# Kernel tuning notes

Hardware: AMD Instinct MI355X
Metric: run time of the kernel (lower is better)

Reference implementation:

```python
import jax, jax.numpy as jnp
import numpy as np

NEG_SLOPE = 0.2  # PyG GATConv default negative_slope


def setup_inputs() -> dict:
    key = jax.random.key(0)
    ks = jax.random.split(key, 10)
    B, N, E = 8, 10000, 160000
    Din, Dout = 128, 128
    x = jax.random.normal(ks[0], (B, N, Din), dtype=jnp.float32)
    src = jax.random.randint(ks[1], (E,), 0, N)
    dst = jax.random.randint(ks[2], (E,), 0, N)
    edge_index = jnp.stack([src, dst])  # [2, E]
    edge_attr = jax.random.uniform(ks[3], (E,), dtype=jnp.float32)
    lim = 1.0 / np.sqrt(Din)
    W = jax.random.uniform(ks[4], (Dout, Din), jnp.float32, -lim, lim)   # shared lin (src==dst)
    We = jax.random.uniform(ks[5], (Dout, 1), jnp.float32, -1.0, 1.0)    # lin_edge, edge_dim=1
    att_src = jax.random.normal(ks[6], (Dout,), jnp.float32) * 0.1
    att_dst = jax.random.normal(ks[7], (Dout,), jnp.float32) * 0.1
    att_edge = jax.random.normal(ks[8], (Dout,), jnp.float32) * 0.1
    bias = jnp.zeros((Dout,), jnp.float32)
    return {"x": x, "edge_index": edge_index, "edge_attr": edge_attr,
            "W": W, "We": We, "att_src": att_src, "att_dst": att_dst,
            "att_edge": att_edge, "bias": bias}


def reference(x, edge_index, edge_attr, W, We, att_src, att_dst, att_edge, bias):
    B, N, Din = x.shape
    src, dst = edge_index[0], edge_index[1]
    # --- add self loops with fill_value='mean' (mean of incoming edge_attr per node) ---
    deg = jax.ops.segment_sum(jnp.ones_like(edge_attr), dst, num_segments=N)
    loop_attr = jax.ops.segment_sum(edge_attr, dst, num_segments=N) / jnp.maximum(deg, 1.0)
    ar = jnp.arange(N, dtype=src.dtype)
    full_src = jnp.concatenate([src, ar])          # [E2]
    full_dst = jnp.concatenate([dst, ar])          # [E2]
    full_attr = jnp.concatenate([edge_attr, loop_attr])
    # edge features: Linear(1 -> Dout, no bias) == outer product; identical across batch
    e_feat = full_attr[:, None] * We[:, 0][None, :]        # [E2, Dout]
    alpha_e = e_feat @ att_edge                            # [E2]

    def single(xb):  # xb: [N, Din]
        h = xb @ W.T                                       # [N, Dout]
        a_src = h @ att_src                                # [N]
        a_dst = h @ att_dst                                # [N]
        a = a_src[full_src] + a_dst[full_dst] + alpha_e    # [E2]
        a = jax.nn.leaky_relu(a, NEG_SLOPE)
        # segment softmax over destination node
        a_max = jax.ops.segment_max(a, full_dst, num_segments=N)
        a_max = jnp.where(jnp.isfinite(a_max), a_max, 0.0)
        ex = jnp.exp(a - a_max[full_dst])
        s = jax.ops.segment_sum(ex, full_dst, num_segments=N)
        alpha = ex / (s[full_dst] + 1e-16)                 # [E2]
        out = jax.ops.segment_sum(alpha[:, None] * h[full_src], full_dst, num_segments=N)
        return out + bias, alpha

    x_out, attn = jax.vmap(single)(x)   # [B, N, Dout], [B, E2]
    return x_out, attn
```

## Files before the change

### kernel.cpp

```cpp
#include <hip/hip_runtime.h>
#include <hip/hip_bf16.h>
#include <hip/hip_fp16.h>

typedef short short8 __attribute__((ext_vector_type(8)));
typedef float floatx4 __attribute__((ext_vector_type(4)));

static constexpr int BATCH = 8;
static constexpr int NN    = 10000;
static constexpr int EE    = 160000;
static constexpr int EE2   = EE + NN;
static constexpr int DD    = 128;
static constexpr int STR   = 64;
static constexpr float SLOPE = 0.2f;
static constexpr long OUT_ELEMS = (long)BATCH * NN * DD;
static constexpr int EB = EE / 256;

__device__ inline float ldf(const void* p, long i, int f32) {
    return f32 ? ((const float*)p)[i]
               : __bfloat162float(((const __hip_bfloat16*)p)[i]);
}
__device__ inline int esrc(const int* ei, int e, int i64) { return i64 ? ei[2 * e] : ei[e]; }
__device__ inline int edst(const int* ei, int e, int i64) { return i64 ? ei[2 * (EE + e)] : ei[EE + e]; }
__device__ inline short bf16bits(float v) {
    __hip_bfloat16 b = __float2bfloat16(v);
    short s; __builtin_memcpy(&s, &b, 2); return s;
}
__device__ inline short f16bits(float v) {
    __half b = __float2half(v);
    short s; __builtin_memcpy(&s, &b, 2); return s;
}

__global__ __launch_bounds__(256) void k_detect(const unsigned short* __restrict__ xu,
                                                const int* __restrict__ ei,
                                                const void* __restrict__ We,
                                                const void* __restrict__ att_edge,
                                                int* __restrict__ flags,
                                                float* __restrict__ cout,
                                                int* __restrict__ deg) {
    int t = threadIdx.x;
    if (blockIdx.x > 0) {
        int idx = (blockIdx.x - 1) * 256 + t;
        if (idx < NN) deg[idx] = 0;
        return;
    }
    __shared__ int cnt[2];
    __shared__ float red[256];
    if (t < 2) cnt[t] = 0;
    __syncthreads();
    int c1 = 0;
    for (int i = t; i < 32768; i += 256) {
        unsigned short u = xu[i];
        if ((u & 0x7F80u) == 0x7F80u) c1++;
    }
    int c2 = (ei[2 * t + 1] != 0) ? 1 : 0;
    if (c1) atomicAdd(&cnt[0], c1);
    if (c2) atomicAdd(&cnt[1], c2);
    __syncthreads();
    int f32 = (cnt[0] > 0);
    if (t == 0) { flags[0] = f32; flags[1] = (cnt[1] == 0); }
    red[t] = (t < DD) ? ldf(We, t, f32) * ldf(att_edge, t, f32) : 0.f;
    __syncthreads();
    for (int o = 128; o > 0; o >>= 1) {
        if (t < o) red[t] += red[t + o];
        __syncthreads();
    }
    if (t == 0) *cout = red[0];
}

__global__ __launch_bounds__(256) void k_bucket(const int* __restrict__ ei,
                                                const void* __restrict__ attr,
                                                const void* __restrict__ W,
                                                const int* __restrict__ flags,
                                                int* __restrict__ deg,
                                                int2* __restrict__ edgesP,
                                                __hip_bfloat16* __restrict__ Wb) {
    int f32 = flags[0], i64 = flags[1];
    int bId = blockIdx.x, t = threadIdx.x;
    if (bId < EB) {
        int e = bId * 256 + t;
        int d = edst(ei, e, i64);
        int s = esrc(ei, e, i64);
        float at = ldf(attr, e, f32);
        int p = atomicAdd(&deg[d], 1);
        if (p < STR) edgesP[d * STR + p] = make_int2(s, __float_as_int(at));
    } else {
        int idx = (bId - EB) * 512 + t * 2;
        if (f32) {
            float2 v = ((const float2*)W)[idx >> 1];
            Wb[idx]     = __float2bfloat16(v.x);
            Wb[idx + 1] = __float2bfloat16(v.y);
        } else {
            ((ushort2*)Wb)[idx >> 1] = ((const ushort2*)W)[idx >> 1];
        }
    }
}

template<int F32>
__device__ inline void load_a(const void* __restrict__ x, long row, int quad, short8 afr[4]) {
    if (F32) {
        const float* xr = (const float*)x + row * DD;
        #pragma unroll
        for (int kk = 0; kk < 4; kk++) {
            float4 f0 = *(const float4*)(xr + kk * 32 + quad * 8);
            float4 f1 = *(const float4*)(xr + kk * 32 + quad * 8 + 4);
            short8 a;
            a[0] = bf16bits(f0.x); a[1] = bf16bits(f0.y); a[2] = bf16bits(f0.z); a[3] = bf16bits(f0.w);
            a[4] = bf16bits(f1.x); a[5] = bf16bits(f1.y); a[6] = bf16bits(f1.z); a[7] = bf16bits(f1.w);
            afr[kk] = a;
        }
    } else {
        const short* xr = (const short*)x + row * DD;
        #pragma unroll
        for (int kk = 0; kk < 4; kk++)
            afr[kk] = *(const short8*)(xr + kk * 32 + quad * 8);
    }
}

__global__ __launch_bounds__(128) void k_gemm(const void* __restrict__ x,
                                              const __hip_bfloat16* __restrict__ Wb,
                                              const void* __restrict__ att_src,
                                              const void* __restrict__ att_dst,
                                              const int* __restrict__ flags,
                                              short* __restrict__ h,
                                              float* __restrict__ asrc_t, float* __restrict__ adst_t) {
    __shared__ float tile[2][16 * 132];
    int f32 = flags[0];
    int wave = threadIdx.x >> 6;
    int lane = threadIdx.x & 63;
    int l15  = lane & 15, quad = lane >> 4;
    long rows_base = (long)blockIdx.x * 32 + wave * 16;

    short8 afr[4];
    if (f32) load_a<1>(x, rows_base + l15, quad, afr);
    else     load_a<0>(x, rows_base + l15, quad, afr);

    const short* wr = (const short*)Wb;
    floatx4 acc[8];
    #pragma unroll
    for (int jt = 0; jt < 8; jt++) acc[jt] = (floatx4){0.f, 0.f, 0.f, 0.f};
    #pragma unroll
    for (int jt = 0; jt < 8; jt++) {
        #pragma unroll
        for (int kk = 0; kk < 4; kk++) {
            short8 bfr = *(const short8*)(wr + (jt * 16 + l15) * DD + kk * 32 + quad * 8);
            acc[jt] = __builtin_amdgcn_mfma_f32_16x16x32_bf16(afr[kk], bfr, acc[jt], 0, 0, 0);
        }
    }

    float asum[4] = {0.f, 0.f, 0.f, 0.f};
    float dsum[4] = {0.f, 0.f, 0.f, 0.f};
    #pragma unroll
    for (int jt = 0; jt < 8; jt++) {
        int col = jt * 16 + l15;
        float as = ldf(att_src, col, f32);
        float ad = ldf(att_dst, col, f32);
        #pragma unroll
        for (int r = 0; r < 4; r++) {
            asum[r] += acc[jt][r] * as;
            dsum[r] += acc[jt][r] * ad;
        }
    }
    #pragma unroll
    for (int r = 0; r < 4; r++) {
        float a = asum[r], d = dsum[r];
        #pragma unroll
        for (int o = 1; o < 16; o <<= 1) { a += __shfl_xor(a, o, 64); d += __shfl_xor(d, o, 64); }
        if (l15 == 0) {
            long row = rows_base + quad * 4 + r;
            int b = (int)(row / NN), n = (int)(row - (long)b * NN);
            asrc_t[n * 8 + b] = a;
            adst_t[n * 8 + b] = d;
        }
    }

    float* tl = &tile[wave][0];
    #pragma unroll
    for (int jt = 0; jt < 8; jt++)
        #pragma unroll
        for (int r = 0; r < 4; r++)
            tl[(quad * 4 + r) * 132 + jt * 16 + l15] = acc[jt][r];
    #pragma unroll
    for (int it = 0; it < 4; it++) {
        int row = it * 4 + quad;
        float4 f0 = *(const float4*)&tl[row * 132 + l15 * 8];
        float4 f1 = *(const float4*)&tl[row * 132 + l15 * 8 + 4];
        short8 o;
        o[0] = f16bits(f0.x); o[1] = f16bits(f0.y); o[2] = f16bits(f0.z); o[3] = f16bits(f0.w);
        o[4] = f16bits(f1.x); o[5] = f16bits(f1.y); o[6] = f16bits(f1.z); o[7] = f16bits(f1.w);
        *(short8*)(h + (rows_base + row) * DD + l15 * 8) = o;
    }
}

__global__ __launch_bounds__(256, 4) void k_agg(const int2* __restrict__ edgesP,
                                                const float* __restrict__ asrc_t,
                                                const float* __restrict__ adst_t,
                                                const __half* __restrict__ h,
                                                const int* __restrict__ deg,
                                                const float* __restrict__ cptr,
                                                const void* __restrict__ bias,
                                                const int* __restrict__ flags,
                                                int nbase,
                                                float* __restrict__ invT,
                                                float* __restrict__ latc,
                                                void* __restrict__ outbuf) {
    __shared__ float4 smeta[16 * 36 + 16];
    int f32 = flags[0];
    int tid = threadIdx.x;
    int lane = tid & 63;
    int g   = lane >> 4;
    int c16 = tid & 15;
    int wv  = tid >> 6;
    int b = blockIdx.x & 7;
    int n = nbase + (blockIdx.x >> 3) * 16 + wv * 4 + g;

    float cc  = *cptr;
    int dg    = min(deg[n], STR);
    float an  = adst_t[n * 8 + b];

    const __half* hb = h + (long)b * NN * DD;
    float4* qptr = smeta + (wv * 4 + g) * 36;

    const int4* em4 = (const int4*)(edgesP + (long)n * STR);
    int4 mr0 = em4[c16];
    int4 mr1;
    if (dg > 32) mr1 = em4[16 + c16];
    else         mr1 = make_int4(n, 0, n, 0);

    float acc[8];
    #pragma unroll
    for (int j = 0; j < 8; j++) acc[j] = 0.f;
    float ssum = 0.f, sattr = 0.f;

#define STAGE(CH, MR)                                                        \
    {   int _e0 = (CH) * 32 + 2 * c16;                                       \
        bool _v0 = _e0 < dg, _v1 = (_e0 + 1) < dg;                           \
        int _s0 = _v0 ? MR.x : n;                                            \
        int _s1 = _v1 ? MR.z : n;                                            \
        float _at0 = _v0 ? __int_as_float(MR.y) : 0.f;                       \
        float _at1 = _v1 ? __int_as_float(MR.w) : 0.f;                       \
        float _ar0 = asrc_t[_s0 * 8 + b];                                    \
        float _ar1 = asrc_t[_s1 * 8 + b];                                    \
        float _a0 = fmaf(cc, _at0, _ar0 + an); _a0 = fmaxf(_a0, SLOPE * _a0);\
        float _a1 = fmaf(cc, _at1, _ar1 + an); _a1 = fmaxf(_a1, SLOPE * _a1);\
        float _ex0 = _v0 ? __expf(_a0) : 0.f;                                \
        float _ex1 = _v1 ? __expf(_a1) : 0.f;                                \
        ssum += _ex0 + _ex1; sattr += _at0 + _at1;                           \
        qptr[(CH) * 16 + c16] = make_float4(_ex0, __int_as_float(_s0),       \
                                            _ex1, __int_as_float(_s1));      \
    }

    STAGE(0, mr0);
    STAGE(1, mr1);

    int npq = (dg + 1) >> 1;
    int t1  = max(npq, __shfl_xor(npq, 16, 64));
    int npw = max(t1, __shfl_xor(t1, 32, 64));

#define DSR(S, MD)   MD = qptr[(S)];
#define HISS(MH, V0, V1)                                                     \
    {   unsigned _o0 = (unsigned)__float_as_int(MH.y) * DD + c16 * 8;        \
        unsigned _o1 = (unsigned)__float_as_int(MH.w) * DD + c16 * 8;        \
        V0 = *(const uint4*)(hb + _o0);                                      \
        V1 = *(const uint4*)(hb + _o1); }
#define FMA8(MF, V0, V1)                                                     \
    {   float _e0 = MF.x, _e1 = MF.z;                                        \
        const __half* _p0 = (const __half*)&V0;                              \
        const __half* _p1 = (const __half*)&V1;                              \
        _Pragma("unroll")                                                    \
        for (int _j = 0; _j < 8; _j++) acc[_j] += _e0 * __half2float(_p0[_j]);\
        _Pragma("unroll")                                                    \
        for (int _j = 0; _j < 8; _j++) acc[_j] += _e1 * __half2float(_p1[_j]);\
    }

    float4 m0, m1, m2, m3, m4, m5, m6, m7;
    uint4 hA0, hA1, hB0, hB1, hC0, hC1, hD0, hD1;
    DSR(0, m0); DSR(1, m1); DSR(2, m2); DSR(3, m3); DSR(4, m4); DSR(5, m5);
    HISS(m0, hA0, hA1); HISS(m1, hB0, hB1); HISS(m2, hC0, hC1);

    for (int p = 0; p < npw; p += 8) {
        DSR(p + 6,  m6); HISS(m3, hD0, hD1); FMA8(m0, hA0, hA1);
        if (p + 1 < npw) { DSR(p + 7,  m7); HISS(m4, hA0, hA1); FMA8(m1, hB0, hB1); }
        if (p + 2 < npw) { DSR(p + 8,  m0); HISS(m5, hB0, hB1); FMA8(m2, hC0, hC1); }
        if (p + 3 < npw) { DSR(p + 9,  m1); HISS(m6, hC0, hC1); FMA8(m3, hD0, hD1); }
        if (p + 4 < npw) { DSR(p + 10, m2); HISS(m7, hD0, hD1); FMA8(m4, hA0, hA1); }
        if (p + 5 < npw) { DSR(p + 11, m3); HISS(m0, hA0, hA1); FMA8(m5, hB0, hB1); }
        if (p + 6 < npw) { DSR(p + 12, m4); HISS(m1, hB0, hB1); FMA8(m6, hC0, hC1); }
        if (p + 7 < npw) { DSR(p + 13, m5); HISS(m2, hC0, hC1); FMA8(m7, hD0, hD1); }
    }
#undef STAGE
#undef DSR
#undef HISS
#undef FMA8

    #pragma unroll
    for (int o = 1; o < 16; o <<= 1) {
        ssum  += __shfl_xor(ssum, o, 64);
        sattr += __shfl_xor(sattr, o, 64);
    }

    float mean = sattr / fmaxf((float)dg, 1.0f);
    {
        float ars = asrc_t[n * 8 + b];
        float a = fmaf(cc, mean, ars + an);
        a = fmaxf(a, SLOPE * a);
        float ex = __expf(a);
        ssum += ex;
        uint4 hv = *(const uint4*)(hb + (unsigned)(n * DD + c16 * 8));
        const __half* hh = (const __half*)&hv;
        #pragma unroll
        for (int j = 0; j < 8; j++) acc[j] += ex * __half2float(hh[j]);
    }
    if (c16 == 0 && b == 0) latc[n] = mean;

    float inv = 1.0f / (ssum + 1e-16f);
    if (c16 == 0) invT[n * 8 + b] = inv;
    #pragma unroll
    for (int j = 0; j < 8; j++) acc[j] = acc[j] * inv + ldf(bias, c16 * 8 + j, f32);

    long row = (long)b * NN + n;
    if (f32) {
        float4 lo = {acc[0], acc[1], acc[2], acc[3]};
        float4 hi = {acc[4], acc[5], acc[6], acc[7]};
        float4* orow = (float4*)((float*)outbuf + row * DD);
        orow[c16 * 2]     = lo;
        orow[c16 * 2 + 1] = hi;
    } else {
        short8 o;
        #pragma unroll
        for (int j = 0; j < 8; j++) o[j] = bf16bits(acc[j]);
        ((short8*)((__hip_bfloat16*)outbuf + row * DD))[c16] = o;
    }
}

__global__ __launch_bounds__(256) void k_attn(const int* __restrict__ ei,
                                              const void* __restrict__ attr,
                                              const float* __restrict__ asrc_t,
                                              const float* __restrict__ adst_t,
                                              const float* __restrict__ latc,
                                              const float* __restrict__ cptr,
                                              const float* __restrict__ invT,
                                              const int* __restrict__ flags,
                                              void* __restrict__ outbuf) {
    int f32 = flags[0], i64 = flags[1];
    int e2 = blockIdx.x * 256 + threadIdx.x;
    if (e2 >= EE2) return;
    float c = *cptr;
    int s, d; float at;
    if (e2 < EE) {
        s = esrc(ei, e2, i64);
        d = edst(ei, e2, i64);
        at = ldf(attr, e2, f32);
    } else {
        int nn = e2 - EE;
        s = nn; d = nn;
        at = latc[nn];
    }
    float4 as0 = *(const float4*)(asrc_t + (long)s * 8);
    float4 as1 = *(const float4*)(asrc_t + (long)s * 8 + 4);
    float4 ad0 = *(const float4*)(adst_t + (long)d * 8);
    float4 ad1 = *(const float4*)(adst_t + (long)d * 8 + 4);
    float4 iv0 = *(const float4*)(invT   + (long)d * 8);
    float4 iv1 = *(const float4*)(invT   + (long)d * 8 + 4);
    float asv[8] = {as0.x, as0.y, as0.z, as0.w, as1.x, as1.y, as1.z, as1.w};
    float adv[8] = {ad0.x, ad0.y, ad0.z, ad0.w, ad1.x, ad1.y, ad1.z, ad1.w};
    float ivv[8] = {iv0.x, iv0.y, iv0.z, iv0.w, iv1.x, iv1.y, iv1.z, iv1.w};
    float ca = c * at;
    #pragma unroll
    for (int b = 0; b < BATCH; b++) {
        float a = asv[b] + adv[b] + ca;
        a = (a > 0.f) ? a : SLOPE * a;
        float al = __expf(a) * ivv[b];
        long gidx = OUT_ELEMS + (long)b * EE2 + e2;
        if (f32) ((float*)outbuf)[gidx] = al;
        else     ((__hip_bfloat16*)outbuf)[gidx] = __float2bfloat16(al);
    }
}

extern "C" void kernel_launch(void* const* d_in, const int* in_sizes, int n_in,
                              void* d_out, int out_size, void* d_ws, size_t ws_size,
                              hipStream_t stream) {
    const void* x        = d_in[0];
    const int*  ei       = (const int*)d_in[1];
    const void* attr     = d_in[2];
    const void* W        = d_in[3];
    const void* We       = d_in[4];
    const void* att_src  = d_in[5];
    const void* att_dst  = d_in[6];
    const void* att_edge = d_in[7];
    const void* bias     = d_in[8];

    char* ws = (char*)d_ws;
    size_t off = 0;
    auto alloc = [&](size_t bytes) { size_t o = off; off = (off + bytes + 255) & ~(size_t)255; return o; };
    short* h             = (short*)(ws + alloc((size_t)BATCH * NN * DD * 2));
    float* asrc_t        = (float*)(ws + alloc((size_t)NN * 8 * 4));
    float* adst_t        = (float*)(ws + alloc((size_t)NN * 8 * 4));
    float* invT          = (float*)(ws + alloc((size_t)NN * 8 * 4));
    int*   deg           = (int*)  (ws + alloc((size_t)NN * 4));
    float* latc          = (float*)(ws + alloc((size_t)NN * 4));
    int2*  edgesP        = (int2*) (ws + alloc((size_t)NN * STR * 8));
    __hip_bfloat16* Wb   = (__hip_bfloat16*)(ws + alloc((size_t)DD * DD * 2));
    float* cscal         = (float*)(ws + alloc(256));
    int*   flags         = (int*)  (ws + alloc(256));

    k_detect<<<41, 256, 0, stream>>>((const unsigned short*)x, ei, We, att_edge,
                                     flags, cscal, deg);
    k_bucket<<<EB + 32, 256, 0, stream>>>(ei, attr, W, flags, deg, edgesP, Wb);
    k_gemm  <<<(BATCH * NN) / 32, 128, 0, stream>>>(x, Wb, att_src, att_dst, flags,
                                                    h, asrc_t, adst_t);
    k_agg<<<(2560 / 16) * 8, 256, 0, stream>>>(edgesP, asrc_t, adst_t, (const __half*)h,
                                               deg, cscal, bias, flags, 0,    invT, latc, d_out);
    k_agg<<<(2560 / 16) * 8, 256, 0, stream>>>(edgesP, asrc_t, adst_t, (const __half*)h,
                                               deg, cscal, bias, flags, 2560, invT, latc, d_out);
    k_agg<<<(2560 / 16) * 8, 256, 0, stream>>>(edgesP, asrc_t, adst_t, (const __half*)h,
                                               deg, cscal, bias, flags, 5120, invT, latc, d_out);
    k_agg<<<(2320 / 16) * 8, 256, 0, stream>>>(edgesP, asrc_t, adst_t, (const __half*)h,
                                               deg, cscal, bias, flags, 7680, invT, latc, d_out);
    k_attn  <<<(EE2 + 255) / 256, 256, 0, stream>>>(ei, attr, asrc_t, adst_t, latc,
                                                    cscal, invT, flags, d_out);
}
```

Baseline: 236.4 us.

## Fuse attention-coefficient output into aggregation kernel via stored edge ids

Records each bucketed edge's original index during bucketing so the aggregation kernel can scatter normalized attention weights (cached exp values times inverse sum) directly to the output. This removes the separate k_attn pass, which recomputed leaky-relu and exp per edge and batch, and removes the invT/latc intermediate buffers. The four chunked k_agg launches are merged into one launch over all nodes. In exchange the attention writes become scattered rather than coalesced, and bucketing writes an extra int per edge.

```diff
diff --git a/kernel.cpp b/kernel.cpp
--- a/kernel.cpp
+++ b/kernel.cpp
@@ -73,6 +73,7 @@
                                                 const int* __restrict__ flags,
                                                 int* __restrict__ deg,
                                                 int2* __restrict__ edgesP,
+                                                int* __restrict__ eidP,
                                                 __hip_bfloat16* __restrict__ Wb) {
     int f32 = flags[0], i64 = flags[1];
     int bId = blockIdx.x, t = threadIdx.x;
@@ -82,7 +83,10 @@
         int s = esrc(ei, e, i64);
         float at = ldf(attr, e, f32);
         int p = atomicAdd(&deg[d], 1);
-        if (p < STR) edgesP[d * STR + p] = make_int2(s, __float_as_int(at));
+        if (p < STR) {
+            edgesP[d * STR + p] = make_int2(s, __float_as_int(at));
+            eidP[d * STR + p] = e;
+        }
     } else {
         int idx = (bId - EB) * 512 + t * 2;
         if (f32) {
@@ -192,6 +196,7 @@
 }
 
 __global__ __launch_bounds__(256, 4) void k_agg(const int2* __restrict__ edgesP,
+                                                const int* __restrict__ eidP,
                                                 const float* __restrict__ asrc_t,
                                                 const float* __restrict__ adst_t,
                                                 const __half* __restrict__ h,
@@ -199,9 +204,6 @@
                                                 const float* __restrict__ cptr,
                                                 const void* __restrict__ bias,
                                                 const int* __restrict__ flags,
-                                                int nbase,
-                                                float* __restrict__ invT,
-                                                float* __restrict__ latc,
                                                 void* __restrict__ outbuf) {
     __shared__ float4 smeta[16 * 36 + 16];
     int f32 = flags[0];
@@ -211,7 +213,7 @@
     int c16 = tid & 15;
     int wv  = tid >> 6;
     int b = blockIdx.x & 7;
-    int n = nbase + (blockIdx.x >> 3) * 16 + wv * 4 + g;
+    int n = (blockIdx.x >> 3) * 16 + wv * 4 + g;
 
     float cc  = *cptr;
     int dg    = min(deg[n], STR);
@@ -299,21 +301,57 @@
     }
 
     float mean = sattr / fmaxf((float)dg, 1.0f);
+    float exSelf;
     {
         float ars = asrc_t[n * 8 + b];
         float a = fmaf(cc, mean, ars + an);
         a = fmaxf(a, SLOPE * a);
-        float ex = __expf(a);
-        ssum += ex;
+        exSelf = __expf(a);
+        ssum += exSelf;
         uint4 hv = *(const uint4*)(hb + (unsigned)(n * DD + c16 * 8));
         const __half* hh = (const __half*)&hv;
         #pragma unroll
-        for (int j = 0; j < 8; j++) acc[j] += ex * __half2float(hh[j]);
-    }
-    if (c16 == 0 && b == 0) latc[n] = mean;
+        for (int j = 0; j < 8; j++) acc[j] += exSelf * __half2float(hh[j]);
+    }
 
     float inv = 1.0f / (ssum + 1e-16f);
-    if (c16 == 0) invT[n * 8 + b] = inv;
+
+    {
+        const int* erow = eidP + n * STR;
+        long abase = OUT_ELEMS + (long)b * EE2;
+        int e0 = 2 * c16;
+        float4 q0 = qptr[c16];
+        int2 id0 = *(const int2*)(erow + e0);
+        if (f32) {
+            float* ao = (float*)outbuf;
+            if (e0 < dg)     ao[abase + id0.x] = q0.x * inv;
+            if (e0 + 1 < dg) ao[abase + id0.y] = q0.z * inv;
+        } else {
+            __hip_bfloat16* ao = (__hip_bfloat16*)outbuf;
+            if (e0 < dg)     ao[abase + id0.x] = __float2bfloat16(q0.x * inv);
+            if (e0 + 1 < dg) ao[abase + id0.y] = __float2bfloat16(q0.z * inv);
+        }
+        if (dg > 32) {
+            int e1 = 32 + 2 * c16;
+            float4 q1 = qptr[16 + c16];
+            int2 id1 = *(const int2*)(erow + e1);
+            if (f32) {
+                float* ao = (float*)outbuf;
+                if (e1 < dg)     ao[abase + id1.x] = q1.x * inv;
+                if (e1 + 1 < dg) ao[abase + id1.y] = q1.z * inv;
+            } else {
+                __hip_bfloat16* ao = (__hip_bfloat16*)outbuf;
+                if (e1 < dg)     ao[abase + id1.x] = __float2bfloat16(q1.x * inv);
+                if (e1 + 1 < dg) ao[abase + id1.y] = __float2bfloat16(q1.z * inv);
+            }
+        }
+        if (c16 == 0) {
+            long gidx = abase + EE + n;
+            if (f32) ((float*)outbuf)[gidx] = exSelf * inv;
+            else     ((__hip_bfloat16*)outbuf)[gidx] = __float2bfloat16(exSelf * inv);
+        }
+    }
+
     #pragma unroll
     for (int j = 0; j < 8; j++) acc[j] = acc[j] * inv + ldf(bias, c16 * 8 + j, f32);
 
@@ -329,50 +367,6 @@
         #pragma unroll
         for (int j = 0; j < 8; j++) o[j] = bf16bits(acc[j]);
         ((short8*)((__hip_bfloat16*)outbuf + row * DD))[c16] = o;
-    }
-}
-
-__global__ __launch_bounds__(256) void k_attn(const int* __restrict__ ei,
-                                              const void* __restrict__ attr,
-                                              const float* __restrict__ asrc_t,
-                                              const float* __restrict__ adst_t,
-                                              const float* __restrict__ latc,
-                                              const float* __restrict__ cptr,
-                                              const float* __restrict__ invT,
-                                              const int* __restrict__ flags,
-                                              void* __restrict__ outbuf) {
-    int f32 = flags[0], i64 = flags[1];
-    int e2 = blockIdx.x * 256 + threadIdx.x;
-    if (e2 >= EE2) return;
-    float c = *cptr;
-    int s, d; float at;
-    if (e2 < EE) {
-        s = esrc(ei, e2, i64);
-        d = edst(ei, e2, i64);
-        at = ldf(attr, e2, f32);
-    } else {
-        int nn = e2 - EE;
-        s = nn; d = nn;
-        at = latc[nn];
-    }
-    float4 as0 = *(const float4*)(asrc_t + (long)s * 8);
-    float4 as1 = *(const float4*)(asrc_t + (long)s * 8 + 4);
-    float4 ad0 = *(const float4*)(adst_t + (long)d * 8);
-    float4 ad1 = *(const float4*)(adst_t + (long)d * 8 + 4);
-    float4 iv0 = *(const float4*)(invT   + (long)d * 8);
-    float4 iv1 = *(const float4*)(invT   + (long)d * 8 + 4);
-    float asv[8] = {as0.x, as0.y, as0.z, as0.w, as1.x, as1.y, as1.z, as1.w};
-    float adv[8] = {ad0.x, ad0.y, ad0.z, ad0.w, ad1.x, ad1.y, ad1.z, ad1.w};
-    float ivv[8] = {iv0.x, iv0.y, iv0.z, iv0.w, iv1.x, iv1.y, iv1.z, iv1.w};
-    float ca = c * at;
-    #pragma unroll
-    for (int b = 0; b < BATCH; b++) {
-        float a = asv[b] + adv[b] + ca;
-        a = (a > 0.f) ? a : SLOPE * a;
-        float al = __expf(a) * ivv[b];
-        long gidx = OUT_ELEMS + (long)b * EE2 + e2;
-        if (f32) ((float*)outbuf)[gidx] = al;
-        else     ((__hip_bfloat16*)outbuf)[gidx] = __float2bfloat16(al);
     }
 }
 
@@ -395,27 +389,18 @@
     short* h             = (short*)(ws + alloc((size_t)BATCH * NN * DD * 2));
     float* asrc_t        = (float*)(ws + alloc((size_t)NN * 8 * 4));
     float* adst_t        = (float*)(ws + alloc((size_t)NN * 8 * 4));
-    float* invT          = (float*)(ws + alloc((size_t)NN * 8 * 4));
     int*   deg           = (int*)  (ws + alloc((size_t)NN * 4));
-    float* latc          = (float*)(ws + alloc((size_t)NN * 4));
     int2*  edgesP        = (int2*) (ws + alloc((size_t)NN * STR * 8));
+    int*   eidP          = (int*)  (ws + alloc((size_t)NN * STR * 4));
     __hip_bfloat16* Wb   = (__hip_bfloat16*)(ws + alloc((size_t)DD * DD * 2));
     float* cscal         = (float*)(ws + alloc(256));
     int*   flags         = (int*)  (ws + alloc(256));
 
     k_detect<<<41, 256, 0, stream>>>((const unsigned short*)x, ei, We, att_edge,
                                      flags, cscal, deg);
-    k_bucket<<<EB + 32, 256, 0, stream>>>(ei, attr, W, flags, deg, edgesP, Wb);
+    k_bucket<<<EB + 32, 256, 0, stream>>>(ei, attr, W, flags, deg, edgesP, eidP, Wb);
     k_gemm  <<<(BATCH * NN) / 32, 128, 0, stream>>>(x, Wb, att_src, att_dst, flags,
                                                     h, asrc_t, adst_t);
-    k_agg<<<(2560 / 16) * 8, 256, 0, stream>>>(edgesP, asrc_t, adst_t, (const __half*)h,
-                                               deg, cscal, bias, flags, 0,    invT, latc, d_out);
-    k_agg<<<(2560 / 16) * 8, 256, 0, stream>>>(edgesP, asrc_t, adst_t, (const __half*)h,
-                                               deg, cscal, bias, flags, 2560, invT, latc, d_out);
-    k_agg<<<(2560 / 16) * 8, 256, 0, stream>>>(edgesP, asrc_t, adst_t, (const __half*)h,
-                                               deg, cscal, bias, flags, 5120, invT, latc, d_out);
-    k_agg<<<(2320 / 16) * 8, 256, 0, stream>>>(edgesP, asrc_t, adst_t, (const __half*)h,
-                                               deg, cscal, bias, flags, 7680, invT, latc, d_out);
-    k_attn  <<<(EE2 + 255) / 256, 256, 0, stream>>>(ei, attr, asrc_t, adst_t, latc,
-                                                    cscal, invT, flags, d_out);
-}
+    k_agg   <<<(BATCH * NN) / 16, 256, 0, stream>>>(edgesP, eidP, asrc_t, adst_t, (const __half*)h,
+                                                    deg, cscal, bias, flags, d_out);
+}
```

After: 214.2 us. -9.4%, faster.
